# Performance work log

Measured on AMD Instinct MI355X. Metric: run time of the kernel, lower is better.

The kernel has to match this reference:

```python
import jax, jax.numpy as jnp
import numpy as np

B = 256
INPUT_DIM = 78464
PC_DIM = 1936
K = 9          # number of step1 sub-models
C = 600        # features per sub-model


def setup_inputs() -> dict:
    key = jax.random.key(0)
    ks = jax.random.split(key, 8)
    x = jax.random.normal(ks[0], (B, INPUT_DIM + 2), dtype=jnp.float32)
    center = jax.random.normal(ks[1], (INPUT_DIM,), dtype=jnp.float32)
    rotation = jax.random.normal(ks[2], (INPUT_DIM, PC_DIM), dtype=jnp.float32) * 0.01
    feats = jax.random.randint(ks[3], (K, C), 0, PC_DIM + 2, dtype=jnp.int32)
    w1 = jax.random.normal(ks[4], (K, C), dtype=jnp.float32) * 0.05   # stacked Linear(C,1) weights
    b1 = jax.random.normal(ks[5], (K,), dtype=jnp.float32)            # stacked biases
    w2 = jax.random.normal(ks[6], (K + 2,), dtype=jnp.float32) * 0.1  # step2 weight
    b2 = jax.random.normal(ks[7], (1,), dtype=jnp.float32)            # step2 bias
    return dict(x=x, center=center, rotation=rotation, feats=feats,
                w1=w1, b1=b1, w2=w2, b2=b2)


def reference(x, center, rotation, feats, w1, b1, w2, b2):
    age = x[:, -1]      # [B]
    female = x[:, -2]   # [B]
    # PCA projection: center and rotate
    p = (x[:, :-2] - center) @ rotation                    # [B, PC_DIM]
    p = jnp.concatenate([p, female[:, None], age[:, None]], axis=1)  # [B, PC_DIM+2]
    # Fused gather + batched tiny GEMMs: 9 Linear(C,1) layers in one einsum
    g = p[:, feats]                                        # [B, K, C]
    s = jnp.einsum('bkc,kc->bk', g, w1) + b1               # [B, K]
    feat2 = jnp.concatenate([s, age[:, None], female[:, None]], axis=1)  # [B, K+2]
    return feat2 @ w2[:, None] + b2                        # [B, 1]
```

## Files before the change

### kernel.cpp

```cpp
#include <hip/hip_runtime.h>

#define IDIM   78464
#define XCOLS  78466
#define PCD    1936
#define PCD2   1938
#define KK     9
#define CC     600
#define BB     256

#define WS_V    0
#define WS_SUMS 2048
#define WS_U    4096

__global__ void k0_zero(float* ws) {
    int i = blockIdx.x * blockDim.x + threadIdx.x;
    if (i < PCD2) ws[WS_V + i] = 0.0f;
}

__global__ void k1_scatter(const int* __restrict__ feats, const float* __restrict__ w1,
                           const float* __restrict__ w2, float* ws) {
    int t = blockIdx.x * blockDim.x + threadIdx.x;
    if (t < KK * CC) {
        int k = t / CC;
        atomicAdd(&ws[WS_V + feats[t]], w2[k] * w1[t]);
    }
}

__global__ __launch_bounds__(256) void k2_matvec(const float* __restrict__ rot,
                                                 const float* __restrict__ v_in,
                                                 float* __restrict__ u) {
    __shared__ __align__(16) float vlds[PCD];
    for (int i = threadIdx.x; i < PCD; i += 256) vlds[i] = v_in[i];
    __syncthreads();

    const int wave = threadIdx.x >> 6;
    const int lane = threadIdx.x & 63;
    const int nw   = gridDim.x << 2;
    const float4* v4 = reinterpret_cast<const float4*>(vlds);

    for (int row = (blockIdx.x << 2) + wave; row < IDIM; row += nw) {
        const float4* r4 = reinterpret_cast<const float4*>(rot + (size_t)row * PCD);
        float ax = 0.f, ay = 0.f, az = 0.f, aw = 0.f;
        #pragma unroll
        for (int it = 0; it < 7; ++it) {
            int j = lane + (it << 6);
            float4 a = r4[j];
            float4 b = v4[j];
            ax += a.x * b.x; ay += a.y * b.y; az += a.z * b.z; aw += a.w * b.w;
        }
        {
            int j = lane + 448;
            if (j < PCD / 4) {
                float4 a = r4[j];
                float4 b = v4[j];
                ax += a.x * b.x; ay += a.y * b.y; az += a.z * b.z; aw += a.w * b.w;
            }
        }
        float s = (ax + ay) + (az + aw);
        #pragma unroll
        for (int off = 32; off; off >>= 1) s += __shfl_down(s, off, 64);
        if (lane == 0) u[row] = s;
    }
}

__global__ __launch_bounds__(1024) void k3_rowdot(const float* __restrict__ x,
                                                  const float* __restrict__ center,
                                                  const float* __restrict__ u,
                                                  float* __restrict__ sums) {
    __shared__ float wred[16];
    const int b = blockIdx.x;
    const float* row = (b < BB) ? (x + (size_t)b * XCOLS) : center;
    const float2* r2 = reinterpret_cast<const float2*>(row);
    const float2* u2 = reinterpret_cast<const float2*>(u);
    float ax = 0.f, ay = 0.f;
    for (int j = threadIdx.x; j < IDIM / 2; j += 1024) {
        float2 a = r2[j];
        float2 c = u2[j];
        ax += a.x * c.x; ay += a.y * c.y;
    }
    float s = ax + ay;
    #pragma unroll
    for (int off = 32; off; off >>= 1) s += __shfl_down(s, off, 64);
    const int wave = threadIdx.x >> 6;
    const int lane = threadIdx.x & 63;
    if (lane == 0) wred[wave] = s;
    __syncthreads();
    if (threadIdx.x == 0) {
        float t = 0.f;
        #pragma unroll
        for (int w = 0; w < 16; ++w) t += wred[w];
        sums[b] = t;
    }
}

__global__ void k4_final(const float* __restrict__ x, const float* __restrict__ b1,
                         const float* __restrict__ w2, const float* __restrict__ b2,
                         const float* __restrict__ ws, float* __restrict__ out) {
    int b = threadIdx.x;
    if (b < BB) {
        float female = x[(size_t)b * XCOLS + IDIM];
        float age    = x[(size_t)b * XCOLS + IDIM + 1];
        float cu     = ws[WS_SUMS + 256];
        float cst = b2[0];
        #pragma unroll
        for (int k = 0; k < KK; ++k) cst += b1[k] * w2[k];
        float r = ws[WS_SUMS + b] - cu
                + female * (ws[WS_V + 1936] + w2[10])
                + age    * (ws[WS_V + 1937] + w2[9])
                + cst;
        out[b] = r;
    }
}

extern "C" void kernel_launch(void* const* d_in, const int* in_sizes, int n_in,
                              void* d_out, int out_size, void* d_ws, size_t ws_size,
                              hipStream_t stream) {
    const float* x      = (const float*)d_in[0];
    const float* center = (const float*)d_in[1];
    const float* rot    = (const float*)d_in[2];
    const int*   feats  = (const int*)  d_in[3];
    const float* w1     = (const float*)d_in[4];
    const float* b1     = (const float*)d_in[5];
    const float* w2     = (const float*)d_in[6];
    const float* b2     = (const float*)d_in[7];
    float* ws  = (float*)d_ws;
    float* out = (float*)d_out;

    hipLaunchKernelGGL(k0_zero,    dim3(8),    dim3(256),  0, stream, ws);
    hipLaunchKernelGGL(k1_scatter, dim3(22),   dim3(256),  0, stream, feats, w1, w2, ws);
    hipLaunchKernelGGL(k2_matvec,  dim3(2048), dim3(256),  0, stream, rot, ws + WS_V, ws + WS_U);
    hipLaunchKernelGGL(k3_rowdot,  dim3(257),  dim3(1024), 0, stream, x, center, ws + WS_U, ws + WS_SUMS);
    hipLaunchKernelGGL(k4_final,   dim3(1),    dim3(256),  0, stream, x, b1, w2, b2, ws, out);
}
```

Before: 151.6 us.

## Split row dots into chunks, fuse v build in LDS, use nontemporal loads

```diff
diff --git a/kernel.cpp b/kernel.cpp
--- a/kernel.cpp
+++ b/kernel.cpp
@@ -7,23 +7,29 @@
 #define KK     9
 #define CC     600
 #define BB     256
+#define CH     8
+#define CHLEN  (IDIM / CH / 2)
+
+typedef float f4 __attribute__((ext_vector_type(4)));
+typedef float f2 __attribute__((ext_vector_type(2)));
 
 #define WS_V    0
-#define WS_SUMS 2048
-#define WS_U    4096
+#define WS_P    2048
+#define WS_U    8192
 
-__global__ void k0_zero(float* ws) {
-    int i = blockIdx.x * blockDim.x + threadIdx.x;
-    if (i < PCD2) ws[WS_V + i] = 0.0f;
-}
-
-__global__ void k1_scatter(const int* __restrict__ feats, const float* __restrict__ w1,
-                           const float* __restrict__ w2, float* ws) {
-    int t = blockIdx.x * blockDim.x + threadIdx.x;
-    if (t < KK * CC) {
+__global__ __launch_bounds__(1024) void k1_buildv(const int* __restrict__ feats,
+                                                  const float* __restrict__ w1,
+                                                  const float* __restrict__ w2,
+                                                  float* __restrict__ v) {
+    __shared__ float vl[PCD2];
+    for (int i = threadIdx.x; i < PCD2; i += 1024) vl[i] = 0.0f;
+    __syncthreads();
+    for (int t = threadIdx.x; t < KK * CC; t += 1024) {
         int k = t / CC;
-        atomicAdd(&ws[WS_V + feats[t]], w2[k] * w1[t]);
+        atomicAdd(&vl[feats[t]], w2[k] * w1[t]);
     }
+    __syncthreads();
+    for (int i = threadIdx.x; i < PCD2; i += 1024) v[i] = vl[i];
 }
 
 __global__ __launch_bounds__(256) void k2_matvec(const float* __restrict__ rot,
@@ -36,23 +42,23 @@
     const int wave = threadIdx.x >> 6;
     const int lane = threadIdx.x & 63;
     const int nw   = gridDim.x << 2;
-    const float4* v4 = reinterpret_cast<const float4*>(vlds);
+    const f4* v4 = reinterpret_cast<const f4*>(vlds);
 
     for (int row = (blockIdx.x << 2) + wave; row < IDIM; row += nw) {
-        const float4* r4 = reinterpret_cast<const float4*>(rot + (size_t)row * PCD);
+        const f4* r4 = reinterpret_cast<const f4*>(rot + (size_t)row * PCD);
         float ax = 0.f, ay = 0.f, az = 0.f, aw = 0.f;
         #pragma unroll
         for (int it = 0; it < 7; ++it) {
             int j = lane + (it << 6);
-            float4 a = r4[j];
-            float4 b = v4[j];
+            f4 a = __builtin_nontemporal_load(&r4[j]);
+            f4 b = v4[j];
             ax += a.x * b.x; ay += a.y * b.y; az += a.z * b.z; aw += a.w * b.w;
         }
         {
             int j = lane + 448;
             if (j < PCD / 4) {
-                float4 a = r4[j];
-                float4 b = v4[j];
+                f4 a = __builtin_nontemporal_load(&r4[j]);
+                f4 b = v4[j];
                 ax += a.x * b.x; ay += a.y * b.y; az += a.z * b.z; aw += a.w * b.w;
             }
         }
@@ -63,20 +69,23 @@
     }
 }
 
-__global__ __launch_bounds__(1024) void k3_rowdot(const float* __restrict__ x,
+__global__ __launch_bounds__(256) void k3_partial(const float* __restrict__ x,
                                                   const float* __restrict__ center,
                                                   const float* __restrict__ u,
-                                                  float* __restrict__ sums) {
-    __shared__ float wred[16];
-    const int b = blockIdx.x;
+                                                  float* __restrict__ part) {
+    __shared__ float wred[4];
+    const int bid = blockIdx.x;
+    const int b = bid >> 3;
+    const int c = bid & (CH - 1);
     const float* row = (b < BB) ? (x + (size_t)b * XCOLS) : center;
-    const float2* r2 = reinterpret_cast<const float2*>(row);
-    const float2* u2 = reinterpret_cast<const float2*>(u);
+    const f2* r2 = reinterpret_cast<const f2*>(row);
+    const f2* u2 = reinterpret_cast<const f2*>(u);
+    const int j0 = c * CHLEN;
     float ax = 0.f, ay = 0.f;
-    for (int j = threadIdx.x; j < IDIM / 2; j += 1024) {
-        float2 a = r2[j];
-        float2 c = u2[j];
-        ax += a.x * c.x; ay += a.y * c.y;
+    for (int j = j0 + threadIdx.x; j < j0 + CHLEN; j += 256) {
+        f2 a = __builtin_nontemporal_load(&r2[j]);
+        f2 uu = u2[j];
+        ax += a.x * uu.x; ay += a.y * uu.y;
     }
     float s = ax + ay;
     #pragma unroll
@@ -85,30 +94,32 @@
     const int lane = threadIdx.x & 63;
     if (lane == 0) wred[wave] = s;
     __syncthreads();
-    if (threadIdx.x == 0) {
-        float t = 0.f;
-        #pragma unroll
-        for (int w = 0; w < 16; ++w) t += wred[w];
-        sums[b] = t;
-    }
+    if (threadIdx.x == 0) part[bid] = (wred[0] + wred[1]) + (wred[2] + wred[3]);
 }
 
-__global__ void k4_final(const float* __restrict__ x, const float* __restrict__ b1,
-                         const float* __restrict__ w2, const float* __restrict__ b2,
-                         const float* __restrict__ ws, float* __restrict__ out) {
+__global__ __launch_bounds__(256) void k4_final(const float* __restrict__ x,
+                                                const float* __restrict__ b1,
+                                                const float* __restrict__ w2,
+                                                const float* __restrict__ b2,
+                                                const float* __restrict__ ws,
+                                                float* __restrict__ out) {
     int b = threadIdx.x;
     if (b < BB) {
         float female = x[(size_t)b * XCOLS + IDIM];
         float age    = x[(size_t)b * XCOLS + IDIM + 1];
-        float cu     = ws[WS_SUMS + 256];
+        float s = 0.f, cu = 0.f;
+        #pragma unroll
+        for (int c = 0; c < CH; ++c) {
+            s  += ws[WS_P + b * CH + c];
+            cu += ws[WS_P + BB * CH + c];
+        }
         float cst = b2[0];
         #pragma unroll
         for (int k = 0; k < KK; ++k) cst += b1[k] * w2[k];
-        float r = ws[WS_SUMS + b] - cu
-                + female * (ws[WS_V + 1936] + w2[10])
-                + age    * (ws[WS_V + 1937] + w2[9])
-                + cst;
-        out[b] = r;
+        out[b] = s - cu
+               + female * (ws[WS_V + 1936] + w2[10])
+               + age    * (ws[WS_V + 1937] + w2[9])
+               + cst;
     }
 }
 
@@ -126,9 +137,8 @@
     float* ws  = (float*)d_ws;
     float* out = (float*)d_out;
 
-    hipLaunchKernelGGL(k0_zero,    dim3(8),    dim3(256),  0, stream, ws);
-    hipLaunchKernelGGL(k1_scatter, dim3(22),   dim3(256),  0, stream, feats, w1, w2, ws);
-    hipLaunchKernelGGL(k2_matvec,  dim3(2048), dim3(256),  0, stream, rot, ws + WS_V, ws + WS_U);
-    hipLaunchKernelGGL(k3_rowdot,  dim3(257),  dim3(1024), 0, stream, x, center, ws + WS_U, ws + WS_SUMS);
-    hipLaunchKernelGGL(k4_final,   dim3(1),    dim3(256),  0, stream, x, b1, w2, b2, ws, out);
+    hipLaunchKernelGGL(k1_buildv,  dim3(1),        dim3(1024), 0, stream, feats, w1, w2, ws + WS_V);
+    hipLaunchKernelGGL(k2_matvec,  dim3(2048),     dim3(256),  0, stream, rot, ws + WS_V, ws + WS_U);
+    hipLaunchKernelGGL(k3_partial, dim3(257 * CH), dim3(256),  0, stream, x, center, ws + WS_U, ws + WS_P);
+    hipLaunchKernelGGL(k4_final,   dim3(1),        dim3(256),  0, stream, x, b1, w2, b2, ws, out);
 }
```

Measured after the change: 137.0 us. 9.6% less time.
